# Performance work log

Measured on AMD Instinct MI355X. Metric: run time of the kernel, lower is better.

## Reference

```python
import jax, jax.numpy as jnp
import numpy as np

WS = 7            # window_size
NUM_HEAD = 8      # dim_in // dim_head = 256 // 32
DIM_HEAD = 32
DIM_IN = 256
DIM_EXP = 1024    # dim_in * exp_ratio(4)


def _ln_c(x, g, b, eps=1e-5):
    # 'ln_1d' norm: LayerNorm over the channel dim for each (b,h,w) position
    m = jnp.mean(x, axis=1, keepdims=True)
    v = jnp.mean((x - m) ** 2, axis=1, keepdims=True)
    return (x - m) * jax.lax.rsqrt(v + eps) * g[None, :, None, None] + b[None, :, None, None]


def _rel_index(ws):
    # static numpy computation identical to the torch buffer construction
    coords = np.stack(np.meshgrid(np.arange(ws), np.arange(ws), indexing='ij'))
    cf = coords.reshape(2, -1)
    rel = (cf[:, :, None] - cf[:, None, :]).transpose(1, 2, 0).astype(np.int64)
    rel[:, :, 0] += ws - 1
    rel[:, :, 1] += ws - 1
    rel[:, :, 0] *= 2 * ws - 1
    return rel.sum(-1)  # (ws*ws, ws*ws)


def setup_inputs() -> dict:
    key = jax.random.key(0)
    ks = jax.random.split(key, 6)
    B, C, H, W = 32, DIM_IN, 56, 56
    win_num = (H // WS) * (W // WS)  # 64 == window_num init arg (required by the reshape)
    return {
        "x": jax.random.normal(ks[0], (B, C, H, W), jnp.float32),
        "pre_g": jnp.ones((C,), jnp.float32),
        "pre_b": jnp.zeros((C,), jnp.float32),
        "post_g": jnp.ones((DIM_EXP // 2,), jnp.float32),
        "post_b": jnp.zeros((DIM_EXP // 2,), jnp.float32),
        "qk_w": jax.random.normal(ks[1], (2 * C, C), jnp.float32) * 0.05,
        "qk_b": jnp.zeros((2 * C,), jnp.float32),
        "v_w": jax.random.normal(ks[2], (DIM_EXP, C), jnp.float32) * 0.05,
        "v_b": jnp.zeros((DIM_EXP,), jnp.float32),
        "proj_w": jax.random.normal(ks[3], (C, DIM_EXP), jnp.float32) * 0.03,
        "proj_b": jnp.zeros((C,), jnp.float32),
        "rpb_table": jax.random.normal(ks[4], (win_num, (2 * WS - 1) ** 2, NUM_HEAD), jnp.float32) * 0.02,
    }


def reference(x, pre_g, pre_b, post_g, post_b, qk_w, qk_b, v_w, v_b, proj_w, proj_b, rpb_table):
    B, C, H, W = x.shape
    n1, n2 = H // WS, W // WS   # H,W divisible by WS -> the pad branch is a no-op
    N = WS * WS
    vh = DIM_EXP // 2 // NUM_HEAD  # v head dim (64)
    shortcut = x
    # dilated window partition: 'b c (h1 n1) (w1 n2) -> (b n1 n2) c h1 w1'
    # NOTE: h1 is the OUTER factor, so each window samples pixels spaced n1/n2 apart.
    xw = x.reshape(B, C, WS, n1, WS, n2).transpose(0, 3, 5, 1, 2, 4).reshape(B * n1 * n2, C, WS, WS)
    xw = _ln_c(xw, pre_g, pre_b)
    b = xw.shape[0]
    # 1x1 convs as GEMMs
    qk = jnp.einsum('bchw,oc->bohw', xw, qk_w) + qk_b[None, :, None, None]
    qk = qk.reshape(b, 2, NUM_HEAD, DIM_HEAD, N).transpose(1, 0, 2, 4, 3)  # (2,b,h,N,dh)
    q, k = qk[0], qk[1]
    v = jnp.einsum('bchw,oc->bohw', xw, v_w) + v_b[None, :, None, None]
    v_attn, v_idle = v[:, :DIM_EXP // 2], v[:, DIM_EXP // 2:]
    v_attn = v_attn.reshape(b, NUM_HEAD, vh, N).transpose(0, 1, 3, 2)      # (b,h,N,vh)
    # relative-position bias gather (per-window table, window_num == n1*n2)
    rel_idx = _rel_index(WS).reshape(-1)                                   # static (N*N,)
    bias = rpb_table[:, rel_idx, :].reshape(n1 * n2, N, N, NUM_HEAD).transpose(0, 3, 1, 2)
    bias = jnp.broadcast_to(bias[None], (B, n1 * n2, NUM_HEAD, N, N)).reshape(b, NUM_HEAD, N, N)
    # SDPA with additive mask; torch SDPA default scale = dim_head**-0.5
    scores = jnp.einsum('bhnd,bhmd->bhnm', q, k) * (DIM_HEAD ** -0.5) + bias
    attn = jax.nn.softmax(scores, axis=-1)
    o = jnp.einsum('bhnm,bhmv->bhnv', attn, v_attn)                        # (b,h,N,vh)
    o = o.transpose(0, 1, 3, 2).reshape(b, DIM_EXP // 2, WS, WS)
    o = _ln_c(o, post_g, post_b)
    xcat = jnp.concatenate([o, v_idle], axis=1)                            # (b,DIM_EXP,WS,WS)
    # window merge: '(b n1 n2) c h1 w1 -> b c (h1 n1) (w1 n2)'
    xm = xcat.reshape(B, n1, n2, DIM_EXP, WS, WS).transpose(0, 3, 4, 1, 5, 2).reshape(B, DIM_EXP, H, W)
    xm = jax.nn.gelu(xm, approximate=False)  # torch nn.GELU default = exact erf
    out = jnp.einsum('bchw,oc->bohw', xm, proj_w) + proj_b[None, :, None, None]
    out = shortcut + out
    return jnp.roll(out, shift=(2, 2), axis=(2, 3))
```

## Files before the change

### kernel.cpp

```cpp
#include <hip/hip_runtime.h>
#include <math.h>

using bf16 = __bf16;
using bf16x8 = __attribute__((ext_vector_type(8))) __bf16;
using f32x4 = __attribute__((ext_vector_type(4))) float;

static __device__ __forceinline__ int imin(int a, int b) { return a < b ? a : b; }
static __device__ __forceinline__ uint32_t swz(int row, uint32_t colb) {
  return colb ^ (uint32_t)((row & 7) << 4);
}
static __device__ __forceinline__ float gelu_f(float v) {
  return 0.5f * v * (1.0f + erff(v * 0.7071067811865475f));
}

__global__ void conv_w_kernel(const float* __restrict__ qk_w,
                              const float* __restrict__ v_w,
                              const float* __restrict__ proj_w,
                              bf16* __restrict__ wqkv,
                              bf16* __restrict__ wproj) {
  int i = blockIdx.x * 256 + threadIdx.x;
  if (i < 131072)       wqkv[i] = (bf16)qk_w[i];
  else if (i < 393216)  wqkv[i] = (bf16)v_w[i - 131072];
  else if (i < 655360)  wproj[i - 393216] = (bf16)proj_w[i - 393216];
}

__global__ void __launch_bounds__(512, 2)
irmb_main(const float* __restrict__ x,
          const float* __restrict__ pre_g,  const float* __restrict__ pre_b,
          const float* __restrict__ post_g, const float* __restrict__ post_b,
          const float* __restrict__ qk_bias, const float* __restrict__ v_bias,
          const float* __restrict__ proj_bias, const float* __restrict__ rpb,
          const bf16* __restrict__ wqkv, const bf16* __restrict__ wproj,
          float* __restrict__ out)
{
  extern __shared__ char smem[];
  char* Abase = smem;
  char* ATT   = smem + 32768;
  char* R2    = smem + 90112;
  char* XMb   = smem + 32768;

  const int tid  = threadIdx.x;
  const int lane = tid & 63;
  const int wv   = tid >> 6;
  const int l15  = lane & 15;
  const int g4   = lane >> 4;
  const int wid  = (blockIdx.x & 7) * 256 + (blockIdx.x >> 3);
  const int bb   = wid >> 6;
  const int wi   = wid & 63;
  const int n1   = wi >> 3, n2 = wi & 7;
  const f32x4 fzero = {0.f, 0.f, 0.f, 0.f};

  {
    const int p8 = tid >> 3;
    const int sub = tid & 7;
    float vals[32];
    float s = 0.f, s2 = 0.f;
    if (p8 < 49) {
      const int r = p8 / 7, c = p8 - r * 7;
      const int hh = r * 8 + n1, ww = c * 8 + n2;
      const float* xp = x + (size_t)bb * 256 * 3136 + hh * 56 + ww;
      #pragma unroll
      for (int j = 0; j < 32; ++j) {
        float v = xp[(size_t)(sub * 32 + j) * 3136];
        vals[j] = v; s += v; s2 += v * v;
      }
    } else {
      #pragma unroll
      for (int j = 0; j < 32; ++j) vals[j] = 0.f;
    }
    #pragma unroll
    for (int m = 1; m < 8; m <<= 1) { s += __shfl_xor(s, m, 64); s2 += __shfl_xor(s2, m, 64); }
    const float mean = s * (1.f / 256.f);
    const float rstd = rsqrtf(s2 * (1.f / 256.f) - mean * mean + 1e-5f);
    #pragma unroll
    for (int q = 0; q < 4; ++q) {
      bf16x8 pk;
      #pragma unroll
      for (int j = 0; j < 8; ++j) {
        const int ch = sub * 32 + q * 8 + j;
        float nv = 0.f;
        if (p8 < 49) nv = (vals[q * 8 + j] - mean) * rstd * pre_g[ch] + pre_b[ch];
        pk[j] = (bf16)nv;
      }
      *(bf16x8*)(Abase + p8 * 512 + swz(p8, (uint32_t)(sub * 64 + q * 16))) = pk;
    }
  }
  __syncthreads();

  {
    const int cb = wv * 64;
    f32x4 acc[4][4];
    #pragma unroll
    for (int i = 0; i < 4; ++i)
      #pragma unroll
      for (int j = 0; j < 4; ++j) acc[i][j] = fzero;
    for (int ks = 0; ks < 8; ++ks) {
      const int kb = ks * 32 + g4 * 8;
      bf16x8 af[4];
      #pragma unroll
      for (int mt = 0; mt < 4; ++mt) {
        const int row = mt * 16 + l15;
        af[mt] = *(const bf16x8*)(Abase + row * 512 + swz(row, (uint32_t)(kb * 2)));
      }
      #pragma unroll
      for (int nt = 0; nt < 4; ++nt) {
        const int col = cb + nt * 16 + l15;
        const bf16x8 bfv = *(const bf16x8*)(wqkv + (size_t)col * 256 + kb);
        #pragma unroll
        for (int mt = 0; mt < 4; ++mt)
          acc[mt][nt] = __builtin_amdgcn_mfma_f32_16x16x32_bf16(af[mt], bfv, acc[mt][nt], 0, 0, 0);
      }
    }
    #pragma unroll
    for (int nt = 0; nt < 4; ++nt) {
      const int ch = cb + nt * 16 + l15;
      const float qb = qk_bias[ch];
      const int sel = ch >> 8, head = (ch >> 5) & 7, d = ch & 31;
      char* base = R2 + head * 7168;
      const uint32_t colb = (uint32_t)((sel * 32 + d) * 2);
      #pragma unroll
      for (int mt = 0; mt < 4; ++mt)
        #pragma unroll
        for (int r = 0; r < 4; ++r) {
          const int n = mt * 16 + g4 * 4 + r;
          if (n < 56) *(bf16*)(base + n * 128 + swz(n, colb)) = (bf16)(acc[mt][nt][r] + qb);
        }
    }
  }
  __syncthreads();

  {
    const int h = wv;
    const char* QK = R2 + h * 7168;
    char* at = ATT + h * 7168;
    f32x4 sa[4][4];
    #pragma unroll
    for (int i = 0; i < 4; ++i)
      #pragma unroll
      for (int j = 0; j < 4; ++j) sa[i][j] = fzero;
    const int kq = g4 * 8;
    bf16x8 qf[4];
    #pragma unroll
    for (int mt = 0; mt < 4; ++mt) {
      const int row = imin(mt * 16 + l15, 55);
      qf[mt] = *(const bf16x8*)(QK + row * 128 + swz(row, (uint32_t)(kq * 2)));
    }
    #pragma unroll
    for (int nt = 0; nt < 4; ++nt) {
      const int mrow = imin(nt * 16 + l15, 55);
      const bf16x8 kf = *(const bf16x8*)(QK + mrow * 128 + swz(mrow, (uint32_t)(64 + kq * 2)));
      #pragma unroll
      for (int mt = 0; mt < 4; ++mt)
        sa[mt][nt] = __builtin_amdgcn_mfma_f32_16x16x32_bf16(qf[mt], kf, sa[mt][nt], 0, 0, 0);
    }
    #pragma unroll
    for (int mt = 0; mt < 4; ++mt)
      #pragma unroll
      for (int r = 0; r < 4; ++r) {
        const int n = mt * 16 + g4 * 4 + r;
        const int rn = n / 7, cn = n - rn * 7;
        float v[4];
        #pragma unroll
        for (int nt = 0; nt < 4; ++nt) {
          const int m = nt * 16 + l15;
          float sv = sa[mt][nt][r] * 0.17677669529663687f;
          if (n < 49 && m < 49) {
            const int rm = m / 7, cm = m - rm * 7;
            sv += rpb[((size_t)wi * 169 + (size_t)((rn - rm + 6) * 13 + (cn - cm + 6))) * 8 + h];
          } else {
            sv = -1e30f;
          }
          v[nt] = sv;
        }
        float mx = fmaxf(fmaxf(v[0], v[1]), fmaxf(v[2], v[3]));
        #pragma unroll
        for (int mm = 1; mm < 16; mm <<= 1) mx = fmaxf(mx, __shfl_xor(mx, mm, 64));
        float sum = 0.f;
        #pragma unroll
        for (int nt = 0; nt < 4; ++nt) { v[nt] = expf(v[nt] - mx); sum += v[nt]; }
        #pragma unroll
        for (int mm = 1; mm < 16; mm <<= 1) sum += __shfl_xor(sum, mm, 64);
        const float inv = 1.f / sum;
        #pragma unroll
        for (int nt = 0; nt < 4; ++nt)
          if (n < 56) *(bf16*)(at + n * 128 + swz(n, (uint32_t)((nt * 16 + l15) * 2))) = (bf16)(v[nt] * inv);
      }
  }
  __syncthreads();

  {
    const int h = wv;
    f32x4 acc[4][4];
    #pragma unroll
    for (int i = 0; i < 4; ++i)
      #pragma unroll
      for (int j = 0; j < 4; ++j) acc[i][j] = fzero;
    for (int ks = 0; ks < 8; ++ks) {
      const int kb = ks * 32 + g4 * 8;
      bf16x8 af[4];
      #pragma unroll
      for (int mt = 0; mt < 4; ++mt) {
        const int row = mt * 16 + l15;
        af[mt] = *(const bf16x8*)(Abase + row * 512 + swz(row, (uint32_t)(kb * 2)));
      }
      #pragma unroll
      for (int nt = 0; nt < 4; ++nt) {
        const int col = 512 + h * 64 + nt * 16 + l15;
        const bf16x8 bfv = *(const bf16x8*)(wqkv + (size_t)col * 256 + kb);
        #pragma unroll
        for (int mt = 0; mt < 4; ++mt)
          acc[mt][nt] = __builtin_amdgcn_mfma_f32_16x16x32_bf16(af[mt], bfv, acc[mt][nt], 0, 0, 0);
      }
    }
    char* V = R2 + h * 8192;
    #pragma unroll
    for (int nt = 0; nt < 4; ++nt) {
      const int vd = nt * 16 + l15;
      const float vb = v_bias[h * 64 + vd];
      #pragma unroll
      for (int mt = 0; mt < 4; ++mt)
        #pragma unroll
        for (int r = 0; r < 4; ++r) {
          const int m = mt * 16 + g4 * 4 + r;
          *(bf16*)(V + vd * 128 + swz(vd, (uint32_t)(m * 2))) = (bf16)(acc[mt][nt][r] + vb);
        }
    }
  }
  __syncthreads();

  f32x4 oacc[4][4];
  {
    const int h = wv;
    const char* at = ATT + h * 7168;
    const char* V = R2 + h * 8192;
    #pragma unroll
    for (int i = 0; i < 4; ++i)
      #pragma unroll
      for (int j = 0; j < 4; ++j) oacc[i][j] = fzero;
    #pragma unroll
    for (int ks = 0; ks < 2; ++ks) {
      const int kb = ks * 32 + g4 * 8;
      bf16x8 af[4];
      #pragma unroll
      for (int mt = 0; mt < 4; ++mt) {
        const int row = imin(mt * 16 + l15, 55);
        af[mt] = *(const bf16x8*)(at + row * 128 + swz(row, (uint32_t)(kb * 2)));
      }
      #pragma unroll
      for (int nt = 0; nt < 4; ++nt) {
        const int vd = nt * 16 + l15;
        const bf16x8 bfv = *(const bf16x8*)(V + vd * 128 + swz(vd, (uint32_t)(kb * 2)));
        #pragma unroll
        for (int mt = 0; mt < 4; ++mt)
          oacc[mt][nt] = __builtin_amdgcn_mfma_f32_16x16x32_bf16(af[mt], bfv, oacc[mt][nt], 0, 0, 0);
      }
    }
  }
  __syncthreads();

  {
    const int h = wv;
    #pragma unroll
    for (int nt = 0; nt < 4; ++nt) {
      const int ch = h * 64 + nt * 16 + l15;
      #pragma unroll
      for (int mt = 0; mt < 4; ++mt)
        #pragma unroll
        for (int r = 0; r < 4; ++r) {
          const int n = mt * 16 + g4 * 4 + r;
          if (n < 56) *(bf16*)(XMb + n * 2048 + swz(n, (uint32_t)(ch * 2))) = (bf16)oacc[mt][nt][r];
        }
    }
  }
  {
    f32x4 acc[4][4];
    #pragma unroll
    for (int i = 0; i < 4; ++i)
      #pragma unroll
      for (int j = 0; j < 4; ++j) acc[i][j] = fzero;
    for (int ks = 0; ks < 8; ++ks) {
      const int kb = ks * 32 + g4 * 8;
      bf16x8 af[4];
      #pragma unroll
      for (int mt = 0; mt < 4; ++mt) {
        const int row = mt * 16 + l15;
        af[mt] = *(const bf16x8*)(Abase + row * 512 + swz(row, (uint32_t)(kb * 2)));
      }
      #pragma unroll
      for (int nt = 0; nt < 4; ++nt) {
        const int fcol = 1024 + wv * 64 + nt * 16 + l15;
        const bf16x8 bfv = *(const bf16x8*)(wqkv + (size_t)fcol * 256 + kb);
        #pragma unroll
        for (int mt = 0; mt < 4; ++mt)
          acc[mt][nt] = __builtin_amdgcn_mfma_f32_16x16x32_bf16(af[mt], bfv, acc[mt][nt], 0, 0, 0);
      }
    }
    #pragma unroll
    for (int nt = 0; nt < 4; ++nt) {
      const int fcol = 1024 + wv * 64 + nt * 16 + l15;
      const int vc = fcol - 512;
      const float vb = v_bias[vc];
      #pragma unroll
      for (int mt = 0; mt < 4; ++mt)
        #pragma unroll
        for (int r = 0; r < 4; ++r) {
          const int n = mt * 16 + g4 * 4 + r;
          if (n < 56) *(bf16*)(XMb + n * 2048 + swz(n, (uint32_t)(vc * 2))) = (bf16)gelu_f(acc[mt][nt][r] + vb);
        }
    }
  }
  __syncthreads();

  {
    const int p8 = tid >> 3, sub = tid & 7;
    float s = 0.f, s2 = 0.f;
    if (p8 < 56) {
      #pragma unroll
      for (int q = 0; q < 8; ++q) {
        const bf16x8 v8 = *(const bf16x8*)(XMb + p8 * 2048 + swz(p8, (uint32_t)(sub * 128 + q * 16)));
        #pragma unroll
        for (int e = 0; e < 8; ++e) { const float v = (float)v8[e]; s += v; s2 += v * v; }
      }
    }
    #pragma unroll
    for (int m = 1; m < 8; m <<= 1) { s += __shfl_xor(s, m, 64); s2 += __shfl_xor(s2, m, 64); }
    const float mean = s * (1.f / 512.f);
    const float rstd = rsqrtf(s2 * (1.f / 512.f) - mean * mean + 1e-5f);
    if (p8 < 56) {
      #pragma unroll
      for (int q = 0; q < 8; ++q) {
        bf16x8* p = (bf16x8*)(XMb + p8 * 2048 + swz(p8, (uint32_t)(sub * 128 + q * 16)));
        bf16x8 v8 = *p;
        #pragma unroll
        for (int e = 0; e < 8; ++e) {
          const int ch = sub * 64 + q * 8 + e;
          const float v = ((float)v8[e] - mean) * rstd * post_g[ch] + post_b[ch];
          v8[e] = (bf16)gelu_f(v);
        }
        *p = v8;
      }
    }
  }
  __syncthreads();

  {
    const int cb = wv * 32;
    f32x4 acc[4][2];
    #pragma unroll
    for (int i = 0; i < 4; ++i)
      #pragma unroll
      for (int j = 0; j < 2; ++j) acc[i][j] = fzero;
    for (int ks = 0; ks < 32; ++ks) {
      const int kb = ks * 32 + g4 * 8;
      bf16x8 af[4];
      #pragma unroll
      for (int mt = 0; mt < 4; ++mt) {
        const int row = imin(mt * 16 + l15, 55);
        af[mt] = *(const bf16x8*)(XMb + row * 2048 + swz(row, (uint32_t)(kb * 2)));
      }
      #pragma unroll
      for (int nt = 0; nt < 2; ++nt) {
        const int col = cb + nt * 16 + l15;
        const bf16x8 bfv = *(const bf16x8*)(wproj + (size_t)col * 1024 + kb);
        #pragma unroll
        for (int mt = 0; mt < 4; ++mt)
          acc[mt][nt] = __builtin_amdgcn_mfma_f32_16x16x32_bf16(af[mt], bfv, acc[mt][nt], 0, 0, 0);
      }
    }
    #pragma unroll
    for (int nt = 0; nt < 2; ++nt) {
      const int oc = cb + nt * 16 + l15;
      const float pb = proj_bias[oc];
      #pragma unroll
      for (int mt = 0; mt < 4; ++mt)
        #pragma unroll
        for (int r = 0; r < 4; ++r) {
          const int n = mt * 16 + g4 * 4 + r;
          if (n < 49) {
            const int rr = n / 7, cc = n - rr * 7;
            const int hh = rr * 8 + n1, ww = cc * 8 + n2;
            const size_t ci = ((size_t)bb * 256 + oc) * 3136;
            const float val = acc[mt][nt][r] + pb + x[ci + hh * 56 + ww];
            int h2 = hh + 2; if (h2 >= 56) h2 -= 56;
            int w2 = ww + 2; if (w2 >= 56) w2 -= 56;
            out[ci + h2 * 56 + w2] = val;
          }
        }
    }
  }
}

extern "C" void kernel_launch(void* const* d_in, const int* in_sizes, int n_in,
                              void* d_out, int out_size, void* d_ws, size_t ws_size,
                              hipStream_t stream) {
  const float* x      = (const float*)d_in[0];
  const float* pre_g  = (const float*)d_in[1];
  const float* pre_b  = (const float*)d_in[2];
  const float* post_g = (const float*)d_in[3];
  const float* post_b = (const float*)d_in[4];
  const float* qk_w   = (const float*)d_in[5];
  const float* qk_b   = (const float*)d_in[6];
  const float* v_w    = (const float*)d_in[7];
  const float* v_b    = (const float*)d_in[8];
  const float* proj_w = (const float*)d_in[9];
  const float* proj_b = (const float*)d_in[10];
  const float* rpb    = (const float*)d_in[11];

  bf16* wqkv  = (bf16*)d_ws;
  bf16* wproj = wqkv + 393216;

  conv_w_kernel<<<2560, 256, 0, stream>>>(qk_w, v_w, proj_w, wqkv, wproj);

  const int smem_bytes = 155648;
  (void)hipFuncSetAttribute((const void*)irmb_main,
                            hipFuncAttributeMaxDynamicSharedMemorySize, smem_bytes);
  irmb_main<<<2048, 512, smem_bytes, stream>>>(
      x, pre_g, pre_b, post_g, post_b, qk_b, v_b, proj_b, rpb,
      wqkv, wproj, (float*)d_out);
}
```

Before: 1.041 ms.

## Double block to 1024 threads, split per-head work across wave pairs, stage RPB in LDS

Each block now runs 16 waves instead of 8. Every GEMM, attention and layernorm stage is re-partitioned so each wave covers half the columns or rows, and two waves share each head. The window's relative position bias table is also copied into shared memory with a per-head transposed layout, so softmax reads it from LDS instead of doing scattered global reads. This aims to hide latency with more waves per CU. In exchange it raises LDS use, lowers per-wave MFMA reuse, and with ~158KB of LDS per block only one block may fit per CU.

```diff
diff --git a/kernel.cpp b/kernel.cpp
--- a/kernel.cpp
+++ b/kernel.cpp
@@ -24,7 +24,7 @@
   else if (i < 655360)  wproj[i - 393216] = (bf16)proj_w[i - 393216];
 }
 
-__global__ void __launch_bounds__(512, 2)
+__global__ void __launch_bounds__(1024, 4)
 irmb_main(const float* __restrict__ x,
           const float* __restrict__ pre_g,  const float* __restrict__ pre_b,
           const float* __restrict__ post_g, const float* __restrict__ post_b,
@@ -38,6 +38,7 @@
   char* ATT   = smem + 32768;
   char* R2    = smem + 90112;
   char* XMb   = smem + 32768;
+  float* RPB  = (float*)(smem + 155648);
 
   const int tid  = threadIdx.x;
   const int lane = tid & 63;
@@ -51,49 +52,53 @@
   const f32x4 fzero = {0.f, 0.f, 0.f, 0.f};
 
   {
-    const int p8 = tid >> 3;
-    const int sub = tid & 7;
-    float vals[32];
+    for (int i = tid; i < 1352; i += 1024) {
+      const int rel = i >> 3, h = i & 7;
+      RPB[h * 176 + rel] = rpb[(size_t)wi * 1352 + i];
+    }
+    const int p8 = tid >> 4;
+    const int sub = tid & 15;
+    float vals[16];
     float s = 0.f, s2 = 0.f;
     if (p8 < 49) {
       const int r = p8 / 7, c = p8 - r * 7;
       const int hh = r * 8 + n1, ww = c * 8 + n2;
       const float* xp = x + (size_t)bb * 256 * 3136 + hh * 56 + ww;
       #pragma unroll
-      for (int j = 0; j < 32; ++j) {
-        float v = xp[(size_t)(sub * 32 + j) * 3136];
+      for (int j = 0; j < 16; ++j) {
+        float v = xp[(size_t)(sub * 16 + j) * 3136];
         vals[j] = v; s += v; s2 += v * v;
       }
     } else {
       #pragma unroll
-      for (int j = 0; j < 32; ++j) vals[j] = 0.f;
-    }
-    #pragma unroll
-    for (int m = 1; m < 8; m <<= 1) { s += __shfl_xor(s, m, 64); s2 += __shfl_xor(s2, m, 64); }
+      for (int j = 0; j < 16; ++j) vals[j] = 0.f;
+    }
+    #pragma unroll
+    for (int m = 1; m < 16; m <<= 1) { s += __shfl_xor(s, m, 64); s2 += __shfl_xor(s2, m, 64); }
     const float mean = s * (1.f / 256.f);
     const float rstd = rsqrtf(s2 * (1.f / 256.f) - mean * mean + 1e-5f);
     #pragma unroll
-    for (int q = 0; q < 4; ++q) {
+    for (int q = 0; q < 2; ++q) {
       bf16x8 pk;
       #pragma unroll
       for (int j = 0; j < 8; ++j) {
-        const int ch = sub * 32 + q * 8 + j;
+        const int ch = sub * 16 + q * 8 + j;
         float nv = 0.f;
         if (p8 < 49) nv = (vals[q * 8 + j] - mean) * rstd * pre_g[ch] + pre_b[ch];
         pk[j] = (bf16)nv;
       }
-      *(bf16x8*)(Abase + p8 * 512 + swz(p8, (uint32_t)(sub * 64 + q * 16))) = pk;
-    }
-  }
-  __syncthreads();
-
-  {
-    const int cb = wv * 64;
-    f32x4 acc[4][4];
+      *(bf16x8*)(Abase + p8 * 512 + swz(p8, (uint32_t)(sub * 32 + q * 16))) = pk;
+    }
+  }
+  __syncthreads();
+
+  {
+    const int cb = wv * 32;
+    f32x4 acc[4][2];
     #pragma unroll
     for (int i = 0; i < 4; ++i)
       #pragma unroll
-      for (int j = 0; j < 4; ++j) acc[i][j] = fzero;
+      for (int j = 0; j < 2; ++j) acc[i][j] = fzero;
     for (int ks = 0; ks < 8; ++ks) {
       const int kb = ks * 32 + g4 * 8;
       bf16x8 af[4];
@@ -103,7 +108,7 @@
         af[mt] = *(const bf16x8*)(Abase + row * 512 + swz(row, (uint32_t)(kb * 2)));
       }
       #pragma unroll
-      for (int nt = 0; nt < 4; ++nt) {
+      for (int nt = 0; nt < 2; ++nt) {
         const int col = cb + nt * 16 + l15;
         const bf16x8 bfv = *(const bf16x8*)(wqkv + (size_t)col * 256 + kb);
         #pragma unroll
@@ -112,7 +117,7 @@
       }
     }
     #pragma unroll
-    for (int nt = 0; nt < 4; ++nt) {
+    for (int nt = 0; nt < 2; ++nt) {
       const int ch = cb + nt * 16 + l15;
       const float qb = qk_bias[ch];
       const int sel = ch >> 8, head = (ch >> 5) & 7, d = ch & 31;
@@ -130,19 +135,20 @@
   __syncthreads();
 
   {
-    const int h = wv;
+    const int h = wv >> 1;
+    const int w2 = wv & 1;
     const char* QK = R2 + h * 7168;
     char* at = ATT + h * 7168;
-    f32x4 sa[4][4];
-    #pragma unroll
-    for (int i = 0; i < 4; ++i)
+    f32x4 sa[2][4];
+    #pragma unroll
+    for (int i = 0; i < 2; ++i)
       #pragma unroll
       for (int j = 0; j < 4; ++j) sa[i][j] = fzero;
     const int kq = g4 * 8;
-    bf16x8 qf[4];
-    #pragma unroll
-    for (int mt = 0; mt < 4; ++mt) {
-      const int row = imin(mt * 16 + l15, 55);
+    bf16x8 qf[2];
+    #pragma unroll
+    for (int mt = 0; mt < 2; ++mt) {
+      const int row = imin((w2 * 2 + mt) * 16 + l15, 55);
       qf[mt] = *(const bf16x8*)(QK + row * 128 + swz(row, (uint32_t)(kq * 2)));
     }
     #pragma unroll
@@ -150,14 +156,14 @@
       const int mrow = imin(nt * 16 + l15, 55);
       const bf16x8 kf = *(const bf16x8*)(QK + mrow * 128 + swz(mrow, (uint32_t)(64 + kq * 2)));
       #pragma unroll
-      for (int mt = 0; mt < 4; ++mt)
+      for (int mt = 0; mt < 2; ++mt)
         sa[mt][nt] = __builtin_amdgcn_mfma_f32_16x16x32_bf16(qf[mt], kf, sa[mt][nt], 0, 0, 0);
     }
     #pragma unroll
-    for (int mt = 0; mt < 4; ++mt)
+    for (int mt = 0; mt < 2; ++mt)
       #pragma unroll
       for (int r = 0; r < 4; ++r) {
-        const int n = mt * 16 + g4 * 4 + r;
+        const int n = (w2 * 2 + mt) * 16 + g4 * 4 + r;
         const int rn = n / 7, cn = n - rn * 7;
         float v[4];
         #pragma unroll
@@ -166,7 +172,7 @@
           float sv = sa[mt][nt][r] * 0.17677669529663687f;
           if (n < 49 && m < 49) {
             const int rm = m / 7, cm = m - rm * 7;
-            sv += rpb[((size_t)wi * 169 + (size_t)((rn - rm + 6) * 13 + (cn - cm + 6))) * 8 + h];
+            sv += RPB[h * 176 + (rn - rm + 6) * 13 + (cn - cm + 6)];
           } else {
             sv = -1e30f;
           }
@@ -189,12 +195,13 @@
   __syncthreads();
 
   {
-    const int h = wv;
-    f32x4 acc[4][4];
+    const int h = wv >> 1;
+    const int w2 = wv & 1;
+    f32x4 acc[4][2];
     #pragma unroll
     for (int i = 0; i < 4; ++i)
       #pragma unroll
-      for (int j = 0; j < 4; ++j) acc[i][j] = fzero;
+      for (int j = 0; j < 2; ++j) acc[i][j] = fzero;
     for (int ks = 0; ks < 8; ++ks) {
       const int kb = ks * 32 + g4 * 8;
       bf16x8 af[4];
@@ -204,8 +211,8 @@
         af[mt] = *(const bf16x8*)(Abase + row * 512 + swz(row, (uint32_t)(kb * 2)));
       }
       #pragma unroll
-      for (int nt = 0; nt < 4; ++nt) {
-        const int col = 512 + h * 64 + nt * 16 + l15;
+      for (int nt = 0; nt < 2; ++nt) {
+        const int col = 512 + h * 64 + w2 * 32 + nt * 16 + l15;
         const bf16x8 bfv = *(const bf16x8*)(wqkv + (size_t)col * 256 + kb);
         #pragma unroll
         for (int mt = 0; mt < 4; ++mt)
@@ -214,8 +221,8 @@
     }
     char* V = R2 + h * 8192;
     #pragma unroll
-    for (int nt = 0; nt < 4; ++nt) {
-      const int vd = nt * 16 + l15;
+    for (int nt = 0; nt < 2; ++nt) {
+      const int vd = w2 * 32 + nt * 16 + l15;
       const float vb = v_bias[h * 64 + vd];
       #pragma unroll
       for (int mt = 0; mt < 4; ++mt)
@@ -228,22 +235,23 @@
   }
   __syncthreads();
 
-  f32x4 oacc[4][4];
-  {
-    const int h = wv;
+  f32x4 oacc[2][4];
+  {
+    const int h = wv >> 1;
+    const int w2 = wv & 1;
     const char* at = ATT + h * 7168;
     const char* V = R2 + h * 8192;
     #pragma unroll
-    for (int i = 0; i < 4; ++i)
+    for (int i = 0; i < 2; ++i)
       #pragma unroll
       for (int j = 0; j < 4; ++j) oacc[i][j] = fzero;
     #pragma unroll
     for (int ks = 0; ks < 2; ++ks) {
       const int kb = ks * 32 + g4 * 8;
-      bf16x8 af[4];
-      #pragma unroll
-      for (int mt = 0; mt < 4; ++mt) {
-        const int row = imin(mt * 16 + l15, 55);
+      bf16x8 af[2];
+      #pragma unroll
+      for (int mt = 0; mt < 2; ++mt) {
+        const int row = imin((w2 * 2 + mt) * 16 + l15, 55);
         af[mt] = *(const bf16x8*)(at + row * 128 + swz(row, (uint32_t)(kb * 2)));
       }
       #pragma unroll
@@ -251,7 +259,7 @@
         const int vd = nt * 16 + l15;
         const bf16x8 bfv = *(const bf16x8*)(V + vd * 128 + swz(vd, (uint32_t)(kb * 2)));
         #pragma unroll
-        for (int mt = 0; mt < 4; ++mt)
+        for (int mt = 0; mt < 2; ++mt)
           oacc[mt][nt] = __builtin_amdgcn_mfma_f32_16x16x32_bf16(af[mt], bfv, oacc[mt][nt], 0, 0, 0);
       }
     }
@@ -259,25 +267,26 @@
   __syncthreads();
 
   {
-    const int h = wv;
+    const int h = wv >> 1;
+    const int w2 = wv & 1;
     #pragma unroll
     for (int nt = 0; nt < 4; ++nt) {
       const int ch = h * 64 + nt * 16 + l15;
       #pragma unroll
-      for (int mt = 0; mt < 4; ++mt)
+      for (int mt = 0; mt < 2; ++mt)
         #pragma unroll
         for (int r = 0; r < 4; ++r) {
-          const int n = mt * 16 + g4 * 4 + r;
+          const int n = (w2 * 2 + mt) * 16 + g4 * 4 + r;
           if (n < 56) *(bf16*)(XMb + n * 2048 + swz(n, (uint32_t)(ch * 2))) = (bf16)oacc[mt][nt][r];
         }
     }
   }
   {
-    f32x4 acc[4][4];
+    f32x4 acc[4][2];
     #pragma unroll
     for (int i = 0; i < 4; ++i)
       #pragma unroll
-      for (int j = 0; j < 4; ++j) acc[i][j] = fzero;
+      for (int j = 0; j < 2; ++j) acc[i][j] = fzero;
     for (int ks = 0; ks < 8; ++ks) {
       const int kb = ks * 32 + g4 * 8;
       bf16x8 af[4];
@@ -287,8 +296,8 @@
         af[mt] = *(const bf16x8*)(Abase + row * 512 + swz(row, (uint32_t)(kb * 2)));
       }
       #pragma unroll
-      for (int nt = 0; nt < 4; ++nt) {
-        const int fcol = 1024 + wv * 64 + nt * 16 + l15;
+      for (int nt = 0; nt < 2; ++nt) {
+        const int fcol = 1024 + wv * 32 + nt * 16 + l15;
         const bf16x8 bfv = *(const bf16x8*)(wqkv + (size_t)fcol * 256 + kb);
         #pragma unroll
         for (int mt = 0; mt < 4; ++mt)
@@ -296,8 +305,8 @@
       }
     }
     #pragma unroll
-    for (int nt = 0; nt < 4; ++nt) {
-      const int fcol = 1024 + wv * 64 + nt * 16 + l15;
+    for (int nt = 0; nt < 2; ++nt) {
+      const int fcol = 1024 + wv * 32 + nt * 16 + l15;
       const int vc = fcol - 512;
       const float vb = v_bias[vc];
       #pragma unroll
@@ -312,28 +321,28 @@
   __syncthreads();
 
   {
-    const int p8 = tid >> 3, sub = tid & 7;
+    const int p8 = tid >> 4, sub = tid & 15;
     float s = 0.f, s2 = 0.f;
     if (p8 < 56) {
       #pragma unroll
-      for (int q = 0; q < 8; ++q) {
-        const bf16x8 v8 = *(const bf16x8*)(XMb + p8 * 2048 + swz(p8, (uint32_t)(sub * 128 + q * 16)));
+      for (int q = 0; q < 4; ++q) {
+        const bf16x8 v8 = *(const bf16x8*)(XMb + p8 * 2048 + swz(p8, (uint32_t)(sub * 64 + q * 16)));
         #pragma unroll
         for (int e = 0; e < 8; ++e) { const float v = (float)v8[e]; s += v; s2 += v * v; }
       }
     }
     #pragma unroll
-    for (int m = 1; m < 8; m <<= 1) { s += __shfl_xor(s, m, 64); s2 += __shfl_xor(s2, m, 64); }
+    for (int m = 1; m < 16; m <<= 1) { s += __shfl_xor(s, m, 64); s2 += __shfl_xor(s2, m, 64); }
     const float mean = s * (1.f / 512.f);
     const float rstd = rsqrtf(s2 * (1.f / 512.f) - mean * mean + 1e-5f);
     if (p8 < 56) {
       #pragma unroll
-      for (int q = 0; q < 8; ++q) {
-        bf16x8* p = (bf16x8*)(XMb + p8 * 2048 + swz(p8, (uint32_t)(sub * 128 + q * 16)));
+      for (int q = 0; q < 4; ++q) {
+        bf16x8* p = (bf16x8*)(XMb + p8 * 2048 + swz(p8, (uint32_t)(sub * 64 + q * 16)));
         bf16x8 v8 = *p;
         #pragma unroll
         for (int e = 0; e < 8; ++e) {
-          const int ch = sub * 64 + q * 8 + e;
+          const int ch = sub * 32 + q * 8 + e;
           const float v = ((float)v8[e] - mean) * rstd * post_g[ch] + post_b[ch];
           v8[e] = (bf16)gelu_f(v);
         }
@@ -344,12 +353,10 @@
   __syncthreads();
 
   {
-    const int cb = wv * 32;
-    f32x4 acc[4][2];
-    #pragma unroll
-    for (int i = 0; i < 4; ++i)
-      #pragma unroll
-      for (int j = 0; j < 2; ++j) acc[i][j] = fzero;
+    const int cb = wv * 16;
+    f32x4 acc[4];
+    #pragma unroll
+    for (int i = 0; i < 4; ++i) acc[i] = fzero;
     for (int ks = 0; ks < 32; ++ks) {
       const int kb = ks * 32 + g4 * 8;
       bf16x8 af[4];
@@ -358,18 +365,14 @@
         const int row = imin(mt * 16 + l15, 55);
         af[mt] = *(const bf16x8*)(XMb + row * 2048 + swz(row, (uint32_t)(kb * 2)));
       }
-      #pragma unroll
-      for (int nt = 0; nt < 2; ++nt) {
-        const int col = cb + nt * 16 + l15;
-        const bf16x8 bfv = *(const bf16x8*)(wproj + (size_t)col * 1024 + kb);
-        #pragma unroll
-        for (int mt = 0; mt < 4; ++mt)
-          acc[mt][nt] = __builtin_amdgcn_mfma_f32_16x16x32_bf16(af[mt], bfv, acc[mt][nt], 0, 0, 0);
-      }
-    }
-    #pragma unroll
-    for (int nt = 0; nt < 2; ++nt) {
-      const int oc = cb + nt * 16 + l15;
+      const int col = cb + l15;
+      const bf16x8 bfv = *(const bf16x8*)(wproj + (size_t)col * 1024 + kb);
+      #pragma unroll
+      for (int mt = 0; mt < 4; ++mt)
+        acc[mt] = __builtin_amdgcn_mfma_f32_16x16x32_bf16(af[mt], bfv, acc[mt], 0, 0, 0);
+    }
+    {
+      const int oc = cb + l15;
       const float pb = proj_bias[oc];
       #pragma unroll
       for (int mt = 0; mt < 4; ++mt)
@@ -380,10 +383,10 @@
             const int rr = n / 7, cc = n - rr * 7;
             const int hh = rr * 8 + n1, ww = cc * 8 + n2;
             const size_t ci = ((size_t)bb * 256 + oc) * 3136;
-            const float val = acc[mt][nt][r] + pb + x[ci + hh * 56 + ww];
+            const float val = acc[mt][r] + pb + x[ci + hh * 56 + ww];
             int h2 = hh + 2; if (h2 >= 56) h2 -= 56;
-            int w2 = ww + 2; if (w2 >= 56) w2 -= 56;
-            out[ci + h2 * 56 + w2] = val;
+            int w2r = ww + 2; if (w2r >= 56) w2r -= 56;
+            out[ci + h2 * 56 + w2r] = val;
           }
         }
     }
@@ -411,10 +414,10 @@
 
   conv_w_kernel<<<2560, 256, 0, stream>>>(qk_w, v_w, proj_w, wqkv, wproj);
 
-  const int smem_bytes = 155648;
+  const int smem_bytes = 161280;
   (void)hipFuncSetAttribute((const void*)irmb_main,
                             hipFuncAttributeMaxDynamicSharedMemorySize, smem_bytes);
-  irmb_main<<<2048, 512, smem_bytes, stream>>>(
+  irmb_main<<<2048, 1024, smem_bytes, stream>>>(
       x, pre_g, pre_b, post_g, post_b, qk_b, v_b, proj_b, rpb,
       wqkv, wproj, (float*)d_out);
 }
```

After: 1.172 ms. 12.6% more time.
